# Kernel optimization log

Measured on AMD Instinct MI355X. Metric: run time of the kernel, lower is better.

## Reference

```python
import jax, jax.numpy as jnp
import numpy as np

D_MODEL = 512
N_HEADS = 8
HEAD_DIM = D_MODEL // N_HEADS
MAX_LEN = 250  # relative table has 2*MAX_LEN-1 = 499 rows
B, L = 2, 2048


def setup_inputs() -> dict:
    rng = jax.random.key(0)
    ks = jax.random.split(rng, 10)
    w = 1.0 / np.sqrt(D_MODEL)
    return {
        "query": jax.random.normal(ks[0], (B, L, D_MODEL), jnp.float32),
        "key": jax.random.normal(ks[1], (B, L, D_MODEL), jnp.float32),
        "value": jax.random.normal(ks[2], (B, L, D_MODEL), jnp.float32),
        "mask": jax.random.randint(ks[3], (B, L), 0, 2, jnp.int32),
        # weights stored as [in, out]; apply as x @ W + b (equivalent to torch Linear)
        "Wq": jax.random.normal(ks[4], (D_MODEL, D_MODEL), jnp.float32) * w,
        "bq": jnp.zeros((D_MODEL,), jnp.float32),
        "Wk": jax.random.normal(ks[5], (D_MODEL, D_MODEL), jnp.float32) * w,
        "bk": jnp.zeros((D_MODEL,), jnp.float32),
        "Wv": jax.random.normal(ks[6], (D_MODEL, D_MODEL), jnp.float32) * w,
        "bv": jnp.zeros((D_MODEL,), jnp.float32),
        "Wo": jax.random.normal(ks[7], (D_MODEL, D_MODEL), jnp.float32) * w,
        "bo": jnp.zeros((D_MODEL,), jnp.float32),
        "rel_table": jax.random.normal(ks[8], (2 * MAX_LEN - 1, HEAD_DIM), jnp.float32),
    }


def reference(query, key, value, mask, Wq, bq, Wk, bk, Wv, bv, Wo, bo, rel_table):
    b, l, d = query.shape
    hd = d // N_HEADS

    def split_heads(x):  # [b,l,d] -> [b,h,l,hd]
        return x.reshape(b, l, N_HEADS, hd).transpose(0, 2, 1, 3)

    Q = split_heads(query @ Wq + bq)
    K = split_heads(key @ Wk + bk)
    V = split_heads(value @ Wv + bv)

    scores = jnp.einsum('bhid,bhjd->bhij', Q, K) / jnp.sqrt(jnp.float32(hd))

    # relative position indices: idx[i,j] = clamp(j - i + MAX_LEN-1, 0, 2*MAX_LEN-2)
    pos = jnp.arange(l)
    idx = jnp.clip(pos[None, :] - pos[:, None] + MAX_LEN - 1, 0, 2 * MAX_LEN - 2)
    rel = rel_table[idx]  # [l, l, hd] gather
    # Shaw-style additive relative-position bias (per-pair scalar from Q . rel)
    scores = scores + jnp.einsum('bhid,ijd->bhij', Q, rel)

    # key-padding mask: [b,l] -> [b,1,1,l]
    scores = jnp.where(mask[:, None, None, :] == 0, jnp.float32(-1e10), scores)

    weights = jax.nn.softmax(scores, axis=-1)  # [b,h,l,l]
    out = jnp.einsum('bhij,bhjd->bhid', weights, V)
    out = out.transpose(0, 2, 1, 3).reshape(b, l, d)
    return out @ Wo + bo
```

## Files before the change

### kernel.cpp

```cpp
#include <hip/hip_runtime.h>
#include <math.h>

#define NREL 499
#define NREL_PAD 500
#define LDB 72
#define LDT 72

typedef __attribute__((ext_vector_type(8))) short bf16x8;
typedef __attribute__((ext_vector_type(4))) float f32x4;

__device__ __forceinline__ float bf2f(ushort x) {
  union { unsigned u; float f; } v; v.u = ((unsigned)x) << 16; return v.f;
}
__device__ __forceinline__ ushort f2bf(float x) {
  union { float f; unsigned u; } v; v.f = x;
  return (ushort)((v.u + 0x8000u) >> 16);
}
__device__ __forceinline__ ushort f2h(float x) {
  union { _Float16 h; ushort u; } v; v.h = (_Float16)x; return v.u;
}
__device__ __forceinline__ float h2f(ushort u) {
  union { _Float16 h; ushort u; } v; v.u = u; return (float)v.h;
}
__device__ __forceinline__ bf16x8 pack8(float4 a, float4 b) {
  bf16x8 r;
  r[0] = (short)f2bf(a.x); r[1] = (short)f2bf(a.y);
  r[2] = (short)f2bf(a.z); r[3] = (short)f2bf(a.w);
  r[4] = (short)f2bf(b.x); r[5] = (short)f2bf(b.y);
  r[6] = (short)f2bf(b.z); r[7] = (short)f2bf(b.w);
  return r;
}

__global__ __launch_bounds__(256) void prep_wt(const float* __restrict__ W0,
                                               const float* __restrict__ W1,
                                               const float* __restrict__ W2,
                                               const float* __restrict__ W3,
                                               const int* __restrict__ mask,
                                               const float* __restrict__ rel,
                                               ushort* __restrict__ Wt,
                                               ushort* __restrict__ maskbf,
                                               ushort* __restrict__ rel8) {
  __shared__ float T[64][68];
  const int t = threadIdx.x;
  const int k0 = blockIdx.x * 64, n0 = blockIdx.y * 64, z = blockIdx.z;
  const float* W = (z == 0) ? W0 : (z == 1) ? W1 : (z == 2) ? W2 : W3;
#pragma unroll
  for (int s = 0; s < 4; ++s) {
    int idx = t + s * 256;
    int r = idx >> 4, c4 = (idx & 15) << 2;
    *(float4*)&T[r][c4] = *(const float4*)(W + (size_t)(k0 + r) * 512 + n0 + c4);
  }
  if (blockIdx.x == 0 && blockIdx.y == 0) {
    int base = z * 1024 + t * 4;
    int4 mv = *(const int4*)(mask + base);
    ushort4 mo;
    mo.x = mv.x ? 0x3F80 : 0; mo.y = mv.y ? 0x3F80 : 0;
    mo.z = mv.z ? 0x3F80 : 0; mo.w = mv.w ? 0x3F80 : 0;
    *(ushort4*)(maskbf + base) = mo;
  } else if (blockIdx.x == 1 && blockIdx.y == 0) {
    int base = z * 8192 + t * 32;
#pragma unroll
    for (int c = 0; c < 4; ++c) {
      int e0 = base + c * 8;
      ushort tmp[8];
#pragma unroll
      for (int k = 0; k < 8; ++k) {
        int e = e0 + k;
        float v = (e < NREL * 64) ? rel[e] * 8.f : 0.f;
        tmp[k] = f2bf(v);
      }
      *(ushort4*)(rel8 + e0) = make_ushort4(tmp[0], tmp[1], tmp[2], tmp[3]);
      *(ushort4*)(rel8 + e0 + 4) = make_ushort4(tmp[4], tmp[5], tmp[6], tmp[7]);
    }
  }
  __syncthreads();
#pragma unroll
  for (int s = 0; s < 4; ++s) {
    int idx = t + s * 256;
    int row = idx >> 4, c4 = (idx & 15) << 2;
    ushort4 u = make_ushort4(f2bf(T[c4 + 0][row]), f2bf(T[c4 + 1][row]),
                             f2bf(T[c4 + 2][row]), f2bf(T[c4 + 3][row]));
    *(ushort4*)(Wt + (size_t)z * 262144 + (size_t)(n0 + row) * 512 + k0 + c4) = u;
  }
}

template <int MODE, int AFP32>
__device__ __forceinline__ void gemm_tile_body(const void* __restrict__ Av,
                                               const ushort* __restrict__ Wt,
                                               const float* __restrict__ bias,
                                               const int* __restrict__ mvec,
                                               void* __restrict__ outv,
                                               int bx, int by, float oscale) {
  __shared__ ushort As[64 * LDT];
  __shared__ ushort Bs[64 * LDT];
  const int t = threadIdx.x;
  const int lane = t & 63, wave = t >> 6;
  const int m16 = lane & 15, quad = lane >> 4;
  const int koff = quad << 3;
  const int i0 = by * 64, n0 = bx * 64;
  const int row0 = t >> 3, off0 = (t & 7) << 3;
  const int row1 = (t + 256) >> 3, off1 = ((t + 256) & 7) << 3;
  const ushort* Ab16 = (const ushort*)Av + (size_t)i0 * 512;
  const float*  Ab32 = (const float*)Av + (size_t)i0 * 512;
  const ushort* Bb = Wt + (size_t)n0 * 512;

  uint4 ar0, ar1;
  float4 af00, af01, af10, af11;
  if (AFP32) {
    af00 = *(const float4*)(Ab32 + (size_t)row0 * 512 + off0);
    af01 = *(const float4*)(Ab32 + (size_t)row0 * 512 + off0 + 4);
    af10 = *(const float4*)(Ab32 + (size_t)row1 * 512 + off1);
    af11 = *(const float4*)(Ab32 + (size_t)row1 * 512 + off1 + 4);
  } else {
    ar0 = *(const uint4*)(Ab16 + (size_t)row0 * 512 + off0);
    ar1 = *(const uint4*)(Ab16 + (size_t)row1 * 512 + off1);
  }
  uint4 br0 = *(const uint4*)(Bb + (size_t)row0 * 512 + off0);
  uint4 br1 = *(const uint4*)(Bb + (size_t)row1 * 512 + off1);

  f32x4 acc[4] = {{0.f, 0.f, 0.f, 0.f}, {0.f, 0.f, 0.f, 0.f},
                  {0.f, 0.f, 0.f, 0.f}, {0.f, 0.f, 0.f, 0.f}};

  for (int ks = 0; ks < 8; ++ks) {
    __syncthreads();
    if (AFP32) {
      *(bf16x8*)&As[row0 * LDT + off0] = pack8(af00, af01);
      *(bf16x8*)&As[row1 * LDT + off1] = pack8(af10, af11);
    } else {
      *(uint4*)&As[row0 * LDT + off0] = ar0;
      *(uint4*)&As[row1 * LDT + off1] = ar1;
    }
    *(uint4*)&Bs[row0 * LDT + off0] = br0;
    *(uint4*)&Bs[row1 * LDT + off1] = br1;
    __syncthreads();

    const int kn = ((ks + 1) & 7) << 6;
    if (AFP32) {
      af00 = *(const float4*)(Ab32 + (size_t)row0 * 512 + kn + off0);
      af01 = *(const float4*)(Ab32 + (size_t)row0 * 512 + kn + off0 + 4);
      af10 = *(const float4*)(Ab32 + (size_t)row1 * 512 + kn + off1);
      af11 = *(const float4*)(Ab32 + (size_t)row1 * 512 + kn + off1 + 4);
    } else {
      ar0 = *(const uint4*)(Ab16 + (size_t)row0 * 512 + kn + off0);
      ar1 = *(const uint4*)(Ab16 + (size_t)row1 * 512 + kn + off1);
    }
    br0 = *(const uint4*)(Bb + (size_t)row0 * 512 + kn + off0);
    br1 = *(const uint4*)(Bb + (size_t)row1 * 512 + kn + off1);

    __builtin_amdgcn_s_setprio(1);
    if (MODE != 1) {
#pragma unroll
      for (int kh = 0; kh < 2; ++kh) {
        bf16x8 af = *(const bf16x8*)&As[((wave << 4) + m16) * LDT + (kh << 5) + koff];
#pragma unroll
        for (int nt = 0; nt < 4; ++nt) {
          bf16x8 wf = *(const bf16x8*)&Bs[((nt << 4) + m16) * LDT + (kh << 5) + koff];
          acc[nt] = __builtin_amdgcn_mfma_f32_16x16x32_bf16(af, wf, acc[nt], 0, 0, 0);
        }
      }
    } else {
#pragma unroll
      for (int kh = 0; kh < 2; ++kh) {
        bf16x8 wf = *(const bf16x8*)&Bs[((wave << 4) + m16) * LDT + (kh << 5) + koff];
#pragma unroll
        for (int it = 0; it < 4; ++it) {
          bf16x8 af = *(const bf16x8*)&As[((it << 4) + m16) * LDT + (kh << 5) + koff];
          acc[it] = __builtin_amdgcn_mfma_f32_16x16x32_bf16(wf, af, acc[it], 0, 0, 0);
        }
      }
    }
    __builtin_amdgcn_s_setprio(0);
  }

  if (MODE == 0) {
    float* out = (float*)outv;
#pragma unroll
    for (int nt = 0; nt < 4; ++nt) {
      float bn = bias[n0 + (nt << 4) + m16];
#pragma unroll
      for (int r = 0; r < 4; ++r) {
        int i = i0 + (wave << 4) + (quad << 2) + r;
        out[(size_t)i * 512 + n0 + (nt << 4) + m16] = acc[nt][r] + bn;
      }
    }
  } else if (MODE == 2) {
    ushort* out = (ushort*)outv;
    const int b = i0 >> 11, l0 = i0 & 2047, h = n0 >> 6;
#pragma unroll
    for (int nt = 0; nt < 4; ++nt) {
      float bn = bias[n0 + (nt << 4) + m16];
      int d = (nt << 4) + m16;
#pragma unroll
      for (int r = 0; r < 4; ++r) {
        int il = (wave << 4) + (quad << 2) + r;
        out[((size_t)(b * 8 + h) * 2048 + l0 + il) * 64 + d] =
            f2bf((acc[nt][r] + bn) * oscale);
      }
    }
  } else {
    ushort* out = (ushort*)outv;
    const int b = i0 >> 11, l0 = i0 & 2047, h = n0 >> 6;
    float4 b4 = *(const float4*)(bias + n0 + (wave << 4) + (quad << 2));
    float bb[4] = {b4.x, b4.y, b4.z, b4.w};
    float mkf[4];
#pragma unroll
    for (int it = 0; it < 4; ++it)
      mkf[it] = (mvec[b * 2048 + l0 + (it << 4) + m16] != 0) ? 1.f : 0.f;
#pragma unroll
    for (int r = 0; r < 4; ++r) {
      int d = (wave << 4) + (quad << 2) + r;
#pragma unroll
      for (int it = 0; it < 4; ++it) {
        out[((size_t)(b * 8 + h) * 64 + d) * 2048 + l0 + (it << 4) + m16] =
            f2bf((acc[it][r] + bb[r]) * mkf[it]);
      }
    }
  }
}

template <int MODE, int AFP32>
__global__ __launch_bounds__(256) void gemm_tile(const void* __restrict__ A,
                                                 const ushort* __restrict__ Wt,
                                                 const float* __restrict__ bias,
                                                 void* __restrict__ outv) {
  gemm_tile_body<MODE, AFP32>(A, Wt, bias, nullptr, outv, blockIdx.x,
                              blockIdx.y, 1.f);
}

__global__ __launch_bounds__(256) void gemm_qkv(
    const float* __restrict__ q, const float* __restrict__ k,
    const float* __restrict__ v, const ushort* __restrict__ Wt,
    const float* __restrict__ bq, const float* __restrict__ bk,
    const float* __restrict__ bv, const int* __restrict__ mask,
    ushort* __restrict__ Qw, ushort* __restrict__ Kw, ushort* __restrict__ Vtw) {
  const int z = blockIdx.z;
  if (z == 0) {
    gemm_tile_body<2, 1>(q, Wt, bq, nullptr, (void*)Qw, blockIdx.x, blockIdx.y,
                         0.125f);
  } else if (z == 1) {
    gemm_tile_body<2, 1>(k, Wt + 262144, bk, nullptr, (void*)Kw, blockIdx.x,
                         blockIdx.y, 1.f);
  } else {
    gemm_tile_body<1, 1>(v, Wt + 2 * 262144, bv, mask, (void*)Vtw, blockIdx.x,
                         blockIdx.y, 1.f);
  }
}

__global__ __launch_bounds__(256) void qrel_tile(const ushort* __restrict__ Qw,
                                                 const ushort* __restrict__ rel8,
                                                 ushort* __restrict__ qrelh) {
  __shared__ ushort As[64 * LDT];
  __shared__ ushort Bs[64 * LDT];
  const int t = threadIdx.x;
  const int lane = t & 63, wave = t >> 6;
  const int m16 = lane & 15, quad = lane >> 4;
  const int koff = quad << 3;
  const int r0 = blockIdx.x * 64;
  const int i0 = blockIdx.y * 64;
  const int bh = blockIdx.z;
  const int row0 = t >> 3, off0 = (t & 7) << 3;
  const int row1 = (t + 256) >> 3, off1 = ((t + 256) & 7) << 3;

  *(uint4*)&As[row0 * LDT + off0] =
      *(const uint4*)(Qw + ((size_t)bh * 2048 + i0 + row0) * 64 + off0);
  *(uint4*)&As[row1 * LDT + off1] =
      *(const uint4*)(Qw + ((size_t)bh * 2048 + i0 + row1) * 64 + off1);
  *(uint4*)&Bs[row0 * LDT + off0] =
      *(const uint4*)(rel8 + (size_t)(r0 + row0) * 64 + off0);
  *(uint4*)&Bs[row1 * LDT + off1] =
      *(const uint4*)(rel8 + (size_t)(r0 + row1) * 64 + off1);
  __syncthreads();

  f32x4 acc[4] = {{0.f, 0.f, 0.f, 0.f}, {0.f, 0.f, 0.f, 0.f},
                  {0.f, 0.f, 0.f, 0.f}, {0.f, 0.f, 0.f, 0.f}};
#pragma unroll
  for (int kh = 0; kh < 2; ++kh) {
    bf16x8 af = *(const bf16x8*)&As[((wave << 4) + m16) * LDT + (kh << 5) + koff];
#pragma unroll
    for (int nt = 0; nt < 4; ++nt) {
      bf16x8 wf = *(const bf16x8*)&Bs[((nt << 4) + m16) * LDT + (kh << 5) + koff];
      acc[nt] = __builtin_amdgcn_mfma_f32_16x16x32_bf16(af, wf, acc[nt], 0, 0, 0);
    }
  }

#pragma unroll
  for (int nt = 0; nt < 4; ++nt) {
    int r = r0 + (nt << 4) + m16;
    if (r < NREL_PAD) {
#pragma unroll
      for (int rg = 0; rg < 4; ++rg) {
        int i = i0 + (wave << 4) + (quad << 2) + rg;
        qrelh[((size_t)bh * 2048 + i) * NREL_PAD + r] = f2h(acc[nt][rg]);
      }
    }
  }
}

__device__ __forceinline__ void gather_qv(float qv[4][4],
                                          const ushort* __restrict__ qrow,
                                          float e_lo, float e_hi,
                                          int iq, int iw0, int j0, int quad) {
  if (j0 - iw0 >= 264) {
#pragma unroll
    for (int jt = 0; jt < 4; ++jt)
#pragma unroll
      for (int r = 0; r < 4; ++r) qv[jt][r] = e_hi;
  } else if (iw0 - j0 >= 312) {
#pragma unroll
    for (int jt = 0; jt < 4; ++jt)
#pragma unroll
      for (int r = 0; r < 4; ++r) qv[jt][r] = e_lo;
  } else {
#pragma unroll
    for (int jt = 0; jt < 4; ++jt) {
#pragma unroll
      for (int r = 0; r < 4; ++r) {
        int j = j0 + (jt << 4) + (quad << 2) + r;
        int rr = min(NREL - 1, max(0, j - iq + 249));
        qv[jt][r] = h2f(qrow[rr]);
      }
    }
  }
}

__global__ __launch_bounds__(256) void flash_attn(
    const ushort* __restrict__ Qw, const ushort* __restrict__ Kw,
    const ushort* __restrict__ Vt, const ushort* __restrict__ qrelh,
    const ushort* __restrict__ maskbf, ushort* __restrict__ attnbf) {
  __shared__ ushort QPs[64 * LDB];
  __shared__ ushort Ks[64 * LDB];
  __shared__ ushort Vs[64 * LDB];
  const int t = threadIdx.x;
  const int lane = t & 63, wave = t >> 6;
  const int m16 = lane & 15, quad = lane >> 4;
  const int koff = quad << 3;
  const int bid = ((int)blockIdx.y << 5) + (int)blockIdx.x;
  const int swz = ((bid & 7) << 6) + (bid >> 3);
  const int i0 = (swz & 31) << 6;
  const int bh = swz >> 5;
  const int b = bh >> 3, h = bh & 7;
  const ushort* Qb = Qw + (size_t)bh * 2048 * 64;
  const ushort* Kb = Kw + (size_t)bh * 2048 * 64;
  const ushort* Vb = Vt + (size_t)bh * 64 * 2048;
  const ushort* mbf = maskbf + b * 2048;
  const int iw0 = i0 + (wave << 4);
  const int iq = iw0 + m16;
  const ushort* qrow = qrelh + ((size_t)bh * 2048 + iq) * NREL_PAD;
  const float e_lo = h2f(qrow[0]), e_hi = h2f(qrow[NREL - 1]);

  const int row0 = t >> 3, off0 = (t & 7) << 3;
  const int row1 = (t + 256) >> 3, off1 = ((t + 256) & 7) << 3;

  *(uint4*)&QPs[row0 * LDB + off0] =
      *(const uint4*)(Qb + (size_t)(i0 + row0) * 64 + off0);
  *(uint4*)&QPs[row1 * LDB + off1] =
      *(const uint4*)(Qb + (size_t)(i0 + row1) * 64 + off1);
  __syncthreads();

  bf16x8 qa0 = *(const bf16x8*)&QPs[((wave << 4) + m16) * LDB + koff];
  bf16x8 qa1 = *(const bf16x8*)&QPs[((wave << 4) + m16) * LDB + 32 + koff];

  float m_i = -INFINITY;
  f32x4 oacc[4];
  f32x4 lacc = {0.f, 0.f, 0.f, 0.f};
#pragma unroll
  for (int dt = 0; dt < 4; ++dt) oacc[dt] = (f32x4){0.f, 0.f, 0.f, 0.f};

  uint4 krA0 = *(const uint4*)(Kb + (size_t)row0 * 64 + off0);
  uint4 krA1 = *(const uint4*)(Kb + (size_t)row1 * 64 + off1);
  uint4 vrA0 = *(const uint4*)(Vb + (size_t)row0 * 2048 + off0);
  uint4 vrA1 = *(const uint4*)(Vb + (size_t)row1 * 2048 + off1);
  bf16x8 mfA0 = *(const bf16x8*)(mbf + koff);
  bf16x8 mfA1 = *(const bf16x8*)(mbf + 32 + koff);
  float qvA[4][4];
  gather_qv(qvA, qrow, e_lo, e_hi, iq, iw0, 0, quad);
  uint4 krB0, krB1, vrB0, vrB1;
  bf16x8 mfB0, mfB1;
  float qvB[4][4];

#define FLASH_STEP(KR0, KR1, VR0, VR1, MF0, MF1, QV,                          \
                   KN0, KN1, VN0, VN1, MG0, MG1, QN, JN)                      \
  do {                                                                        \
    __syncthreads();                                                          \
    *(uint4*)&Ks[row0 * LDB + off0] = KR0;                                    \
    *(uint4*)&Ks[row1 * LDB + off1] = KR1;                                    \
    *(uint4*)&Vs[row0 * LDB + off0] = VR0;                                    \
    *(uint4*)&Vs[row1 * LDB + off1] = VR1;                                    \
    __syncthreads();                                                          \
    KN0 = *(const uint4*)(Kb + (size_t)((JN) + row0) * 64 + off0);            \
    KN1 = *(const uint4*)(Kb + (size_t)((JN) + row1) * 64 + off1);            \
    VN0 = *(const uint4*)(Vb + (size_t)row0 * 2048 + (JN) + off0);            \
    VN1 = *(const uint4*)(Vb + (size_t)row1 * 2048 + (JN) + off1);            \
    MG0 = *(const bf16x8*)(mbf + (JN) + koff);                                \
    MG1 = *(const bf16x8*)(mbf + (JN) + 32 + koff);                           \
    gather_qv(QN, qrow, e_lo, e_hi, iq, iw0, (JN), quad);                     \
    f32x4 sacc[4];                                                            \
    __builtin_amdgcn_s_setprio(1);                                            \
    _Pragma("unroll")                                                         \
    for (int jt = 0; jt < 4; ++jt) {                                          \
      bf16x8 kf0 = *(const bf16x8*)&Ks[((jt << 4) + m16) * LDB + koff];       \
      bf16x8 kf1 = *(const bf16x8*)&Ks[((jt << 4) + m16) * LDB + 32 + koff];  \
      f32x4 z = {QV[jt][0], QV[jt][1], QV[jt][2], QV[jt][3]};                 \
      z = __builtin_amdgcn_mfma_f32_16x16x32_bf16(kf0, qa0, z, 0, 0, 0);      \
      z = __builtin_amdgcn_mfma_f32_16x16x32_bf16(kf1, qa1, z, 0, 0, 0);      \
      sacc[jt] = z;                                                           \
    }                                                                         \
    __builtin_amdgcn_s_setprio(0);                                            \
    float t0 = fmaxf(fmaxf(sacc[0][0], sacc[0][1]),                           \
                     fmaxf(sacc[0][2], sacc[0][3]));                          \
    float t1 = fmaxf(fmaxf(sacc[1][0], sacc[1][1]),                           \
                     fmaxf(sacc[1][2], sacc[1][3]));                          \
    float t2 = fmaxf(fmaxf(sacc[2][0], sacc[2][1]),                           \
                     fmaxf(sacc[2][2], sacc[2][3]));                          \
    float t3 = fmaxf(fmaxf(sacc[3][0], sacc[3][1]),                           \
                     fmaxf(sacc[3][2], sacc[3][3]));                          \
    float mx = fmaxf(fmaxf(t0, t1), fmaxf(t2, t3));                           \
    mx = fmaxf(mx, __shfl_xor(mx, 16));                                       \
    mx = fmaxf(mx, __shfl_xor(mx, 32));                                       \
    if (__any(mx > m_i + 8.f)) {                                              \
      float mnew = fmaxf(m_i, mx);                                            \
      float al = __expf(m_i - mnew);                                          \
      m_i = mnew;                                                             \
      _Pragma("unroll")                                                       \
      for (int dt = 0; dt < 4; ++dt) {                                        \
        oacc[dt][0] *= al; oacc[dt][1] *= al;                                 \
        oacc[dt][2] *= al; oacc[dt][3] *= al;                                 \
      }                                                                       \
      lacc[0] *= al; lacc[1] *= al; lacc[2] *= al; lacc[3] *= al;             \
    }                                                                         \
    const int prow = ((wave << 4) + m16) * LDB;                               \
    _Pragma("unroll")                                                         \
    for (int jt = 0; jt < 4; ++jt) {                                          \
      ushort4 pk;                                                             \
      pk.x = f2bf(__expf(sacc[jt][0] - m_i));                                 \
      pk.y = f2bf(__expf(sacc[jt][1] - m_i));                                 \
      pk.z = f2bf(__expf(sacc[jt][2] - m_i));                                 \
      pk.w = f2bf(__expf(sacc[jt][3] - m_i));                                 \
      *(ushort4*)&QPs[prow + (jt << 4) + (quad << 2)] = pk;                   \
    }                                                                         \
    __asm__ volatile("s_waitcnt lgkmcnt(0)" ::: "memory");                    \
    bf16x8 pa0 = *(const bf16x8*)&QPs[prow + koff];                           \
    bf16x8 pa1 = *(const bf16x8*)&QPs[prow + 32 + koff];                      \
    __builtin_amdgcn_s_setprio(1);                                            \
    lacc = __builtin_amdgcn_mfma_f32_16x16x32_bf16(MF0, pa0, lacc, 0, 0, 0);  \
    lacc = __builtin_amdgcn_mfma_f32_16x16x32_bf16(MF1, pa1, lacc, 0, 0, 0);  \
    _Pragma("unroll")                                                         \
    for (int dt = 0; dt < 4; ++dt) {                                          \
      bf16x8 vf0 = *(const bf16x8*)&Vs[((dt << 4) + m16) * LDB + koff];       \
      bf16x8 vf1 = *(const bf16x8*)&Vs[((dt << 4) + m16) * LDB + 32 + koff];  \
      oacc[dt] =                                                              \
          __builtin_amdgcn_mfma_f32_16x16x32_bf16(vf0, pa0, oacc[dt], 0, 0, 0); \
      oacc[dt] =                                                              \
          __builtin_amdgcn_mfma_f32_16x16x32_bf16(vf1, pa1, oacc[dt], 0, 0, 0); \
    }                                                                         \
    __builtin_amdgcn_s_setprio(0);                                            \
  } while (0)

  for (int j0 = 0; j0 < 2048; j0 += 128) {
    FLASH_STEP(krA0, krA1, vrA0, vrA1, mfA0, mfA1, qvA,
               krB0, krB1, vrB0, vrB1, mfB0, mfB1, qvB, j0 + 64);
    FLASH_STEP(krB0, krB1, vrB0, vrB1, mfB0, mfB1, qvB,
               krA0, krA1, vrA0, vrA1, mfA0, mfA1, qvA, (j0 + 128) & 2047);
  }
#undef FLASH_STEP

  float inv = 1.0f / lacc[0];
  ushort* dst = attnbf + (size_t)(b * 2048 + iq) * 512 + h * 64;
#pragma unroll
  for (int dt = 0; dt < 4; ++dt) {
    ushort4 st;
    st.x = f2bf(oacc[dt][0] * inv);
    st.y = f2bf(oacc[dt][1] * inv);
    st.z = f2bf(oacc[dt][2] * inv);
    st.w = f2bf(oacc[dt][3] * inv);
    *(ushort4*)(dst + (dt << 4) + (quad << 2)) = st;
  }
}

extern "C" void kernel_launch(void* const* d_in, const int* in_sizes, int n_in,
                              void* d_out, int out_size, void* d_ws,
                              size_t ws_size, hipStream_t stream) {
  const float* query = (const float*)d_in[0];
  const float* key   = (const float*)d_in[1];
  const float* value = (const float*)d_in[2];
  const int*   mask  = (const int*)d_in[3];
  const float* Wq = (const float*)d_in[4];
  const float* bq = (const float*)d_in[5];
  const float* Wk = (const float*)d_in[6];
  const float* bk = (const float*)d_in[7];
  const float* Wv = (const float*)d_in[8];
  const float* bv = (const float*)d_in[9];
  const float* Wo = (const float*)d_in[10];
  const float* bo = (const float*)d_in[11];
  const float* rel = (const float*)d_in[12];

  char* w = (char*)d_ws;
  size_t off = 0;
  ushort* Qw  = (ushort*)(w + off); off += (size_t)16 * 2048 * 64 * 2;
  ushort* Kw  = (ushort*)(w + off); off += (size_t)16 * 2048 * 64 * 2;
  ushort* Vtw = (ushort*)(w + off); off += (size_t)16 * 64 * 2048 * 2;
  ushort* Wt  = (ushort*)(w + off); off += (size_t)4 * 512 * 512 * 2;
  ushort* qrelh = (ushort*)(w + off); off += (size_t)16 * 2048 * NREL_PAD * 2;
  ushort* attnbf = (ushort*)(w + off); off += (size_t)4096 * 512 * 2;
  ushort* maskbf = (ushort*)(w + off); off += (size_t)2 * 2048 * 2;
  ushort* rel8 = (ushort*)(w + off); off += (size_t)512 * 64 * 2;
  float* out = (float*)d_out;

  dim3 bb(256);
  hipLaunchKernelGGL(prep_wt, dim3(8, 8, 4), bb, 0, stream, Wq, Wk, Wv, Wo,
                     mask, rel, Wt, maskbf, rel8);
  hipLaunchKernelGGL(gemm_qkv, dim3(8, 64, 3), bb, 0, stream, query, key, value,
                     Wt, bq, bk, bv, mask, Qw, Kw, Vtw);
  hipLaunchKernelGGL(qrel_tile, dim3(8, 32, 16), bb, 0, stream, Qw, rel8, qrelh);
  hipLaunchKernelGGL(flash_attn, dim3(32, 16), bb, 0, stream, Qw, Kw, Vtw,
                     qrelh, maskbf, attnbf);
  hipLaunchKernelGGL((gemm_tile<0, 0>), dim3(8, 64), bb, 0, stream, attnbf,
                     Wt + 3 * 262144, bo, (void*)out);
}
```

Before: 212.7 us.

## Use 128-row tiles for Q/K projections and stage qrel stores through LDS

The Q and K projection GEMMs move to a new 128x64 tile routine in which each wave computes two 16-row sub-tiles, so each weight fragment is reused twice and the QKV grid is halved. The V projection block now loops over two 64-row tiles to match the smaller grid. The qrel kernel writes its tile into shared memory and then stores it with 16-byte vector writes, with NREL_PAD raised to 504 so rows stay 16-byte aligned. This trades more LDS use and a larger qrel buffer for more reuse and coalesced stores.

```diff
diff --git a/kernel.cpp b/kernel.cpp
--- a/kernel.cpp
+++ b/kernel.cpp
@@ -2,7 +2,7 @@
 #include <math.h>
 
 #define NREL 499
-#define NREL_PAD 500
+#define NREL_PAD 504
 #define LDB 72
 #define LDT 72
 
@@ -183,20 +183,6 @@
         out[(size_t)i * 512 + n0 + (nt << 4) + m16] = acc[nt][r] + bn;
       }
     }
-  } else if (MODE == 2) {
-    ushort* out = (ushort*)outv;
-    const int b = i0 >> 11, l0 = i0 & 2047, h = n0 >> 6;
-#pragma unroll
-    for (int nt = 0; nt < 4; ++nt) {
-      float bn = bias[n0 + (nt << 4) + m16];
-      int d = (nt << 4) + m16;
-#pragma unroll
-      for (int r = 0; r < 4; ++r) {
-        int il = (wave << 4) + (quad << 2) + r;
-        out[((size_t)(b * 8 + h) * 2048 + l0 + il) * 64 + d] =
-            f2bf((acc[nt][r] + bn) * oscale);
-      }
-    }
   } else {
     ushort* out = (ushort*)outv;
     const int b = i0 >> 11, l0 = i0 & 2047, h = n0 >> 6;
@@ -225,6 +211,97 @@
                                                  void* __restrict__ outv) {
   gemm_tile_body<MODE, AFP32>(A, Wt, bias, nullptr, outv, blockIdx.x,
                               blockIdx.y, 1.f);
+}
+
+__device__ __forceinline__ void gemm_qk128(const float* __restrict__ A,
+                                           const ushort* __restrict__ Wt,
+                                           const float* __restrict__ bias,
+                                           ushort* __restrict__ out,
+                                           int bx, int by, float oscale) {
+  __shared__ ushort As[128 * LDT];
+  __shared__ ushort Bs[64 * LDT];
+  const int t = threadIdx.x;
+  const int lane = t & 63, wave = t >> 6;
+  const int m16 = lane & 15, quad = lane >> 4;
+  const int koff = quad << 3;
+  const int i0 = by * 128, n0 = bx * 64;
+  const float* Ab = A + (size_t)i0 * 512;
+  const ushort* Bb = Wt + (size_t)n0 * 512;
+
+  int arow[4], acol[4];
+#pragma unroll
+  for (int s = 0; s < 4; ++s) {
+    int idx = t + s * 256;
+    arow[s] = idx >> 3;
+    acol[s] = (idx & 7) << 3;
+  }
+  const int brow0 = t >> 3, bcol0 = (t & 7) << 3;
+  const int brow1 = (t + 256) >> 3, bcol1 = ((t + 256) & 7) << 3;
+
+  float4 afA[4], afB[4];
+  uint4 br0, br1;
+#pragma unroll
+  for (int s = 0; s < 4; ++s) {
+    afA[s] = *(const float4*)(Ab + (size_t)arow[s] * 512 + acol[s]);
+    afB[s] = *(const float4*)(Ab + (size_t)arow[s] * 512 + acol[s] + 4);
+  }
+  br0 = *(const uint4*)(Bb + (size_t)brow0 * 512 + bcol0);
+  br1 = *(const uint4*)(Bb + (size_t)brow1 * 512 + bcol1);
+
+  f32x4 acc[2][4];
+#pragma unroll
+  for (int mi = 0; mi < 2; ++mi)
+#pragma unroll
+    for (int nt = 0; nt < 4; ++nt) acc[mi][nt] = (f32x4){0.f, 0.f, 0.f, 0.f};
+
+  for (int ks = 0; ks < 8; ++ks) {
+    __syncthreads();
+#pragma unroll
+    for (int s = 0; s < 4; ++s)
+      *(bf16x8*)&As[arow[s] * LDT + acol[s]] = pack8(afA[s], afB[s]);
+    *(uint4*)&Bs[brow0 * LDT + bcol0] = br0;
+    *(uint4*)&Bs[brow1 * LDT + bcol1] = br1;
+    __syncthreads();
+
+    const int kn = ((ks + 1) & 7) << 6;
+#pragma unroll
+    for (int s = 0; s < 4; ++s) {
+      afA[s] = *(const float4*)(Ab + (size_t)arow[s] * 512 + kn + acol[s]);
+      afB[s] = *(const float4*)(Ab + (size_t)arow[s] * 512 + kn + acol[s] + 4);
+    }
+    br0 = *(const uint4*)(Bb + (size_t)brow0 * 512 + kn + bcol0);
+    br1 = *(const uint4*)(Bb + (size_t)brow1 * 512 + kn + bcol1);
+
+    __builtin_amdgcn_s_setprio(1);
+#pragma unroll
+    for (int kh = 0; kh < 2; ++kh) {
+      bf16x8 af0 = *(const bf16x8*)&As[((wave << 5) + m16) * LDT + (kh << 5) + koff];
+      bf16x8 af1 = *(const bf16x8*)&As[((wave << 5) + 16 + m16) * LDT + (kh << 5) + koff];
+#pragma unroll
+      for (int nt = 0; nt < 4; ++nt) {
+        bf16x8 wf = *(const bf16x8*)&Bs[((nt << 4) + m16) * LDT + (kh << 5) + koff];
+        acc[0][nt] = __builtin_amdgcn_mfma_f32_16x16x32_bf16(af0, wf, acc[0][nt], 0, 0, 0);
+        acc[1][nt] = __builtin_amdgcn_mfma_f32_16x16x32_bf16(af1, wf, acc[1][nt], 0, 0, 0);
+      }
+    }
+    __builtin_amdgcn_s_setprio(0);
+  }
+
+  const int b = i0 >> 11, l0 = i0 & 2047, h = n0 >> 6;
+#pragma unroll
+  for (int nt = 0; nt < 4; ++nt) {
+    float bn = bias[n0 + (nt << 4) + m16];
+    int d = (nt << 4) + m16;
+#pragma unroll
+    for (int mi = 0; mi < 2; ++mi) {
+#pragma unroll
+      for (int r = 0; r < 4; ++r) {
+        int il = (wave << 5) + (mi << 4) + (quad << 2) + r;
+        out[((size_t)(b * 8 + h) * 2048 + l0 + il) * 64 + d] =
+            f2bf((acc[mi][nt][r] + bn) * oscale);
+      }
+    }
+  }
 }
 
 __global__ __launch_bounds__(256) void gemm_qkv(
@@ -235,14 +312,14 @@
     ushort* __restrict__ Qw, ushort* __restrict__ Kw, ushort* __restrict__ Vtw) {
   const int z = blockIdx.z;
   if (z == 0) {
-    gemm_tile_body<2, 1>(q, Wt, bq, nullptr, (void*)Qw, blockIdx.x, blockIdx.y,
-                         0.125f);
+    gemm_qk128(q, Wt, bq, Qw, blockIdx.x, blockIdx.y, 0.125f);
   } else if (z == 1) {
-    gemm_tile_body<2, 1>(k, Wt + 262144, bk, nullptr, (void*)Kw, blockIdx.x,
-                         blockIdx.y, 1.f);
+    gemm_qk128(k, Wt + 262144, bk, Kw, blockIdx.x, blockIdx.y, 1.f);
   } else {
-    gemm_tile_body<1, 1>(v, Wt + 2 * 262144, bv, mask, (void*)Vtw, blockIdx.x,
-                         blockIdx.y, 1.f);
+#pragma unroll
+    for (int s = 0; s < 2; ++s)
+      gemm_tile_body<1, 1>(v, Wt + 2 * 262144, bv, mask, (void*)Vtw,
+                           blockIdx.x, blockIdx.y * 2 + s, 1.f);
   }
 }
 
@@ -283,17 +360,23 @@
     }
   }
 
+  __syncthreads();
 #pragma unroll
   for (int nt = 0; nt < 4; ++nt) {
-    int r = r0 + (nt << 4) + m16;
-    if (r < NREL_PAD) {
-#pragma unroll
-      for (int rg = 0; rg < 4; ++rg) {
-        int i = i0 + (wave << 4) + (quad << 2) + rg;
-        qrelh[((size_t)bh * 2048 + i) * NREL_PAD + r] = f2h(acc[nt][rg]);
-      }
-    }
-  }
+#pragma unroll
+    for (int rg = 0; rg < 4; ++rg) {
+      int il = (wave << 4) + (quad << 2) + rg;
+      As[il * LDT + (nt << 4) + m16] = f2h(acc[nt][rg]);
+    }
+  }
+  __syncthreads();
+
+  const int orow = t >> 2, och = (t & 3) << 4;
+  uint4 s0 = *(const uint4*)&As[orow * LDT + och];
+  uint4 s1 = *(const uint4*)&As[orow * LDT + och + 8];
+  ushort* dst = qrelh + ((size_t)bh * 2048 + i0 + orow) * NREL_PAD + r0 + och;
+  *(uint4*)dst = s0;
+  if (r0 + och + 15 < NREL_PAD) *(uint4*)(dst + 8) = s1;
 }
 
 __device__ __forceinline__ void gather_qv(float qv[4][4],
@@ -509,7 +592,7 @@
   dim3 bb(256);
   hipLaunchKernelGGL(prep_wt, dim3(8, 8, 4), bb, 0, stream, Wq, Wk, Wv, Wo,
                      mask, rel, Wt, maskbf, rel8);
-  hipLaunchKernelGGL(gemm_qkv, dim3(8, 64, 3), bb, 0, stream, query, key, value,
+  hipLaunchKernelGGL(gemm_qkv, dim3(8, 32, 3), bb, 0, stream, query, key, value,
                      Wt, bq, bk, bv, mask, Qw, Kw, Vtw);
   hipLaunchKernelGGL(qrel_tile, dim3(8, 32, 16), bb, 0, stream, Qw, rel8, qrelh);
   hipLaunchKernelGGL(flash_attn, dim3(32, 16), bb, 0, stream, Qw, Kw, Vtw,
```

After: 213.8 us. Within noise of the previous version (+0.5%).
